# Optimization experiments

Measured on AMD Instinct MI355X. Metric: run time of the kernel, lower is better.

Reference implementation:

```python
import jax, jax.numpy as jnp
import numpy as np
from jax import lax

C = 256          # hidden_channels
K_ITERS = 3      # num_iterations

def _conv(x, w, b, stride=1, pad='SAME'):
    y = lax.conv_general_dilated(x, w, (stride, stride), pad,
                                 dimension_numbers=('NCHW', 'OIHW', 'NCHW'))
    return y + b[None, :, None, None]

def setup_inputs() -> dict:
    key = jax.random.key(0)
    ks = jax.random.split(key, 16)
    B, N, H, W = 1, 3, 384, 384
    def p(k, sh, scale=None):
        if scale is None:
            scale = 1.0 / np.sqrt(np.prod(sh[1:]))
        return jax.random.normal(k, sh, jnp.float32) * scale
    z = lambda: jnp.zeros((C,), jnp.float32)
    return {
        'frames': jax.random.normal(ks[0], (B, N, 3, H, W), jnp.float32),
        'backbone_w': p(ks[1], (C, 3, 8, 8)), 'backbone_b': z(),
        'W_intra': p(ks[2], (C, C), scale=1.0 / C),
        'W_inter': p(ks[3], (C, C), scale=1.0 / C),
        'gate_w': p(ks[4], (C, C, 1, 1)), 'gate_b': z(),
        'Wz': p(ks[5], (C, 2 * C, 3, 3)), 'bz': z(),
        'Wr': p(ks[6], (C, 2 * C, 3, 3)), 'br': z(),
        'Wh': p(ks[7], (C, 2 * C, 3, 3)), 'bh': z(),
        'ro_w1': p(ks[8], (C, 2 * C, 3, 3)), 'ro_b1': z(),
        'ro_w2': p(ks[9], (1, C, 3, 3)), 'ro_b2': jnp.zeros((1,), jnp.float32),
    }

def _forward(frames, backbone_w, backbone_b, W_intra, W_inter, gate_w, gate_b,
             Wz, bz, Wr, br, Wh, bh, ro_w1, ro_b1, ro_w2, ro_b2):
    B, N, _, H, W = frames.shape
    x = frames.reshape(B * N, 3, H, W)
    # backbone: stride-8 conv + ReLU -> node embeddings v (B*N, C, Hf, Wf)
    v = jax.nn.relu(_conv(x, backbone_w, backbone_b, stride=8, pad='VALID'))
    Hf, Wf = v.shape[2], v.shape[3]
    P = Hf * Wf
    v = v.reshape(B, N, C, Hf, Wf)
    h = v
    idx = jnp.arange(N)
    for _ in range(K_ITERS):
        hp = h.reshape(B, N, C, P).transpose(0, 1, 3, 2)      # (B,N,P,C)
        # inter attention e_ij = h_i W h_j^T over all ordered pairs
        t = jnp.einsum('bipc,cd->bipd', hp, W_inter)
        e = jnp.einsum('bipd,bjqd->bijpq', t, hp)              # (B,N,N,P,P)
        # intra (loop-edge) attention on the diagonal, own weight
        ti = jnp.einsum('bipc,cd->bipd', hp, W_intra)
        e_intra = jnp.einsum('bipd,biqd->bipq', ti, hp)        # (B,N,P,P)
        e = e.at[:, idx, idx].set(e_intra)
        attn = jax.nn.softmax(e, axis=-1)
        m = jnp.einsum('bijpq,bjqc->bijpc', attn, hp)          # msg j->i (B,N,N,P,C)
        m = m.transpose(0, 1, 2, 4, 3).reshape(B * N * N, C, Hf, Wf)
        # gated aggregation: sigmoid(1x1 conv) gate, sum over senders j
        g = jax.nn.sigmoid(_conv(m, gate_w, gate_b))
        magg = (g * m).reshape(B, N, N, C, Hf, Wf).sum(axis=2).reshape(B * N, C, Hf, Wf)
        # ConvGRU update
        hflat = h.reshape(B * N, C, Hf, Wf)
        mh = jnp.concatenate([magg, hflat], axis=1)
        zg = jax.nn.sigmoid(_conv(mh, Wz, bz))
        rg = jax.nn.sigmoid(_conv(mh, Wr, br))
        hc = jnp.tanh(_conv(jnp.concatenate([magg, rg * hflat], axis=1), Wh, bh))
        h = ((1.0 - zg) * hflat + zg * hc).reshape(B, N, C, Hf, Wf)
    # read-out on concat(h, v)
    cat = jnp.concatenate([h, v], axis=2).reshape(B * N, 2 * C, Hf, Wf)
    y = jax.nn.relu(_conv(cat, ro_w1, ro_b1))
    masks = _conv(y, ro_w2, ro_b2)
    return masks.reshape(B, N, 1, Hf, Wf)

def reference(frames, backbone_w, backbone_b, W_intra, W_inter, gate_w, gate_b,
              Wz, bz, Wr, br, Wh, bh, ro_w1, ro_b1, ro_w2, ro_b2):
    return _forward(frames, backbone_w, backbone_b, W_intra, W_inter, gate_w, gate_b,
                    Wz, bz, Wr, br, Wh, bh, ro_w1, ro_b1, ro_w2, ro_b2)
```

## Files before the change

kernel.cpp:

```cpp
#include <hip/hip_runtime.h>
#include <hip/hip_bf16.h>
#include <math.h>

#define PIX 2304
#define CCH 256
#define CP  589824
#define NCP 1769472
#define KC  4608
#define PADR 2512

typedef __hip_bfloat16 bf16;
typedef __attribute__((ext_vector_type(8))) short bf16x8;
typedef __attribute__((ext_vector_type(4))) float f32x4;

__device__ __forceinline__ float sigmoidf_(float x){ return 1.f/(1.f+__expf(-x)); }

__device__ __forceinline__ void gl_lds16(const bf16* g, bf16* lds){
    __builtin_amdgcn_global_load_lds(
        (const __attribute__((address_space(1))) void*)g,
        (__attribute__((address_space(3))) void*)lds, 16, 0, 0);
}
#define FENCE() asm volatile("" ::: "memory")

__device__ __forceinline__ float bperm_f(int srcLane, float v){
    return __int_as_float(__builtin_amdgcn_ds_bpermute(srcLane<<2, __float_as_int(v)));
}
__device__ __forceinline__ unsigned packbf(float lo, float hi){
    bf16 a = __float2bfloat16(lo), b = __float2bfloat16(hi);
    return (unsigned)(*(unsigned short*)&a) | ((unsigned)(*(unsigned short*)&b)<<16);
}

__global__ __launch_bounds__(512) void fattn_k(
    const bf16* __restrict__ T, const bf16* __restrict__ Ti,
    const bf16* __restrict__ Khp, const bf16* __restrict__ Vcp,
    bf16* __restrict__ Ob)
{
    __shared__ bf16 Ks[2][64*256];
    __shared__ bf16 Vs[2][256*64];
    __shared__ unsigned Ps[8][512];
    const int z = blockIdx.z, i = z/3, j = z%3;
    const bf16* Q  = ((i==j)? Ti : T) + (long)i*CP;
    const bf16* Kp = Khp + (long)j*CP;
    const bf16* Vp = Vcp + (long)j*CP;
    const int tid = threadIdx.x, l = tid & 63, w = tid >> 6;
    const int g = l>>4, m = l&15;
    const int q0 = blockIdx.x*128;

    bf16x8 qf[8];
    {
        const bf16* qr = Q + (long)(q0 + w*16 + m)*256 + g*8;
        #pragma unroll
        for (int ks=0; ks<8; ++ks) qf[ks] = *(const bf16x8*)(qr + ks*32);
    }
    f32x4 oacc[16];
    #pragma unroll
    for (int nf=0; nf<16; ++nf) oacc[nf] = (f32x4){0.f,0.f,0.f,0.f};
    float mrun = -3e38f;
    float lrun = 0.f;

    auto stage = [&](int buf, int t){
        const int kq = t*64;
        #pragma unroll
        for (int u=0; u<4; ++u){
            int idx = u*512 + tid;
            int rr = idx>>5, cc = idx&31;
            gl_lds16(Kp + (long)(kq+rr)*256 + ((cc ^ (rr&7))<<3),
                     &Ks[buf][(u*512 + (tid & ~63))*8]);
        }
        #pragma unroll
        for (int u=0; u<4; ++u){
            int idx = u*512 + tid;
            int rr = idx>>3, cc = idx&7;
            gl_lds16(Vp + (long)rr*2304 + kq + ((cc ^ (rr&7))<<3),
                     &Vs[buf][(u*512 + (tid & ~63))*8]);
        }
    };

    stage(0, 0);
    int cur = 0;
    char* pw = (char*)&Ps[w][0];
    for (int t=0; t<36; ++t){
        if (t+1 < 36){
            stage(cur^1, t+1);
            asm volatile("s_waitcnt vmcnt(8)" ::: "memory");
        } else {
            asm volatile("s_waitcnt vmcnt(0)" ::: "memory");
        }
        __builtin_amdgcn_s_barrier();
        FENCE();

        f32x4 sacc[4];
        #pragma unroll
        for (int nf=0; nf<4; ++nf) sacc[nf] = (f32x4){0.f,0.f,0.f,0.f};
        __builtin_amdgcn_s_setprio(1);
        #pragma unroll
        for (int ks=0; ks<8; ++ks){
            #pragma unroll
            for (int nf=0; nf<4; ++nf){
                int row = nf*16 + m;
                int phys = (ks*4 + g) ^ (row&7);
                bf16x8 kf = *(const bf16x8*)&Ks[cur][row*256 + phys*8];
                sacc[nf] = __builtin_amdgcn_mfma_f32_16x16x32_bf16(kf, qf[ks], sacc[nf], 0,0,0);
            }
        }
        __builtin_amdgcn_s_setprio(0);

        float pmax = -3e38f;
        #pragma unroll
        for (int nf=0; nf<4; ++nf)
            #pragma unroll
            for (int r=0; r<4; ++r) pmax = fmaxf(pmax, sacc[nf][r]);
        pmax = fmaxf(pmax, __shfl_xor(pmax, 16));
        pmax = fmaxf(pmax, __shfl_xor(pmax, 32));
        if (!__all(pmax - mrun <= 8.f)){
            float mn = fmaxf(mrun, pmax);
            float al = __expf(mrun - mn);
            mrun = mn;
            lrun *= al;
            float ar[4];
            #pragma unroll
            for (int r=0; r<4; ++r) ar[r] = bperm_f((l & 48) | (g*4 + r), al);
            #pragma unroll
            for (int nf=0; nf<16; ++nf)
                #pragma unroll
                for (int r=0; r<4; ++r) oacc[nf][r] *= ar[r];
        }
        float rs = 0.f;
        unsigned pk[4][2];
        #pragma unroll
        for (int nf=0; nf<4; ++nf){
            float p0 = __expf(sacc[nf][0] - mrun);
            float p1 = __expf(sacc[nf][1] - mrun);
            float p2 = __expf(sacc[nf][2] - mrun);
            float p3 = __expf(sacc[nf][3] - mrun);
            rs += (p0+p1) + (p2+p3);
            pk[nf][0] = packbf(p0, p1);
            pk[nf][1] = packbf(p2, p3);
        }
        rs += __shfl_xor(rs, 16);
        rs += __shfl_xor(rs, 32);
        lrun += rs;
        #pragma unroll
        for (int nf=0; nf<4; ++nf)
            #pragma unroll
            for (int s=0; s<2; ++s){
                int ba = m*128 + ((nf*32 + g*8 + s*4) ^ ((m&7)<<4));
                *(unsigned*)(pw + ba) = pk[nf][s];
            }
        asm volatile("s_waitcnt lgkmcnt(0)" ::: "memory");
        __builtin_amdgcn_sched_barrier(0);
        __builtin_amdgcn_s_setprio(1);
        #pragma unroll
        for (int ks2=0; ks2<2; ++ks2){
            bf16x8 pa = *(const bf16x8*)(pw + m*128 + ((ks2*64 + g*16) ^ ((m&7)<<4)));
            #pragma unroll
            for (int nf=0; nf<16; ++nf){
                int row = nf*16 + m;
                int phys = (ks2*4 + g) ^ (row&7);
                bf16x8 bv = *(const bf16x8*)&Vs[cur][row*64 + phys*8];
                oacc[nf] = __builtin_amdgcn_mfma_f32_16x16x32_bf16(pa, bv, oacc[nf], 0,0,0);
            }
        }
        __builtin_amdgcn_s_setprio(0);
        FENCE();
        __builtin_amdgcn_s_barrier();
        FENCE();
        cur ^= 1;
    }

    float linv = 1.f / lrun;
    float li[4];
    #pragma unroll
    for (int r=0; r<4; ++r) li[r] = bperm_f((l & 48) | (g*4 + r), linv);
    bf16* ob = Ob + (long)z*CP;
    const int prow0 = q0 + w*16 + g*4;
    #pragma unroll
    for (int nf=0; nf<16; ++nf){
        int c = nf*16 + m;
        #pragma unroll
        for (int r=0; r<4; ++r)
            ob[(long)(prow0+r)*256 + c] = __float2bfloat16(oacc[nf][r]*li[r]);
    }
}

template<int EPI, int BN>
__global__ __launch_bounds__(256) void mgemm_k(
    const bf16* __restrict__ A0, const bf16* __restrict__ A1, int diagz,
    const bf16* __restrict__ B,
    float* __restrict__ o0, bf16* __restrict__ ob,
    const bf16* __restrict__ aux, const float* __restrict__ bias0,
    int M, int N, int lda, int ldb, int ldc, int auxld,
    long bsA, long bsB, long bsC, long bsAux,
    int nzJ, int Ksub, long bsKc)
{
    __shared__ bf16 As[2][128*64];
    __shared__ bf16 Bs[2][BN*64];
    const int z = blockIdx.z;
    const int jz = z % nzJ, kc = z / nzJ;
    const bf16* Ap = ((jz==diagz)?A1:A0) + jz*bsA + (long)blockIdx.x*128*lda;
    const bf16* Bp = B + jz*bsB + (long)blockIdx.y*BN*ldb;
    const int tid = threadIdx.x, l = tid & 63;
    const int wvu = tid & ~63;
    const int wr = tid>>7, wc = (tid>>6)&1;
    constexpr int NF = BN/32;
    f32x4 acc[4][NF];
    #pragma unroll
    for (int i=0;i<4;++i)
        #pragma unroll
        for (int j=0;j<NF;++j) acc[i][j] = (f32x4){0.f,0.f,0.f,0.f};

    auto stage = [&](int buf, int kb){
        #pragma unroll
        for (int u=0;u<4;++u){
            int idx = u*256 + tid;
            int row = idx>>3, g = (idx&7) ^ (row&7);
            gl_lds16(Ap + (long)row*lda + kb + g*8, &As[buf][(u*256+wvu)*8]);
        }
        #pragma unroll
        for (int u=0;u<BN/32;++u){
            int idx = u*256 + tid;
            int row = idx>>3, g = (idx&7) ^ (row&7);
            gl_lds16(Bp + (long)row*ldb + kb + g*8, &Bs[buf][(u*256+wvu)*8]);
        }
    };

    const int kbeg = kc*Ksub;
    const int nk = Ksub >> 6;
    stage(0, kbeg);
    int cur = 0;
    for (int t=0; t<nk; ++t){
        if (t+1 < nk){
            stage(cur^1, kbeg + (t+1)*64);
            if constexpr (BN==64) asm volatile("s_waitcnt vmcnt(6)" ::: "memory");
            else                  asm volatile("s_waitcnt vmcnt(8)" ::: "memory");
        } else {
            asm volatile("s_waitcnt vmcnt(0)" ::: "memory");
        }
        __builtin_amdgcn_s_barrier();
        FENCE();
        #pragma unroll
        for (int ks=0; ks<64; ks+=32){
            bf16x8 af[4], bfr[NF];
            #pragma unroll
            for (int i=0;i<4;++i){
                int row = wr*64 + i*16 + (l&15);
                af[i] = *(const bf16x8*)&As[cur][row*64 + ((((ks>>3)+(l>>4)) ^ (row&7))<<3)];
            }
            #pragma unroll
            for (int j=0;j<NF;++j){
                int row = wc*(BN/2) + j*16 + (l&15);
                bfr[j] = *(const bf16x8*)&Bs[cur][row*64 + ((((ks>>3)+(l>>4)) ^ (row&7))<<3)];
            }
            #pragma unroll
            for (int i=0;i<4;++i)
                #pragma unroll
                for (int j=0;j<NF;++j)
                    acc[i][j] = __builtin_amdgcn_mfma_f32_16x16x32_bf16(af[i], bfr[j], acc[i][j], 0,0,0);
        }
        FENCE();
        __builtin_amdgcn_s_barrier();
        FENCE();
        cur ^= 1;
    }

    const int mb = blockIdx.x*128 + wr*64, nb = blockIdx.y*BN + wc*(BN/2);
    #pragma unroll
    for (int i=0;i<4;++i)
        #pragma unroll
        for (int j=0;j<NF;++j){
            int gm0 = mb + i*16 + ((l>>4)<<2);
            int gn  = nb + j*16 + (l&15);
            #pragma unroll
            for (int r=0;r<4;++r){
                int gm = gm0 + r;
                float vacc = acc[i][j][r];
                if (EPI==0){
                    ob[jz*bsC + (long)gm*ldc + gn] = __float2bfloat16(vacc);
                } else {
                    float g = sigmoidf_(vacc + bias0[gm]);
                    float mv = __bfloat162float(aux[jz*bsAux + (long)gn*auxld + gm]);
                    o0[jz*bsC + (long)gm*ldc + gn] = g*mv;
                }
            }
        }
}

__global__ __launch_bounds__(256) void cgemm2_k(
    const bf16* __restrict__ inpad, const bf16* __restrict__ W,
    float* __restrict__ part, int N)
{
    __shared__ bf16 As[2][128*64];
    __shared__ bf16 Bs[2][64*64];
    const int tid = threadIdx.x, l = tid & 63, wvu = tid & ~63;
    const int wr = tid>>7, wc = (tid>>6)&1;
    const int bx = blockIdx.x, by = blockIdx.y, kc = blockIdx.z;
    const int img = bx/18, m0 = (bx - img*18)*128;
    const bf16* Ab = inpad + (long)img*PADR*512;
    const bf16* Bb = W + (long)by*64*KC;
    f32x4 acc[4][2];
    #pragma unroll
    for (int i=0;i<4;++i){ acc[i][0]=(f32x4){0,0,0,0}; acc[i][1]=(f32x4){0,0,0,0}; }

    auto stageA = [&](int buf, int k0){
        int tap = k0 >> 9, ci0 = k0 & 511;
        int dy = tap/3, dx = tap - 3*dy;
        int shift = (dy-1)*50 + (dx-1);
        #pragma unroll
        for (int u=0;u<4;++u){
            int idx = u*256 + tid;
            int row = idx>>3;
            int om = m0 + row;
            int prow = om + 2*(om/48) + 51 + shift;
            int g = (idx&7) ^ (row&7);
            gl_lds16(Ab + (long)prow*512 + ci0 + g*8, &As[buf][(u*256+wvu)*8]);
        }
    };
    auto stageB = [&](int buf, int k0){
        #pragma unroll
        for (int u=0;u<2;++u){
            int idx = u*256 + tid;
            int row = idx>>3;
            int g = (idx&7) ^ (row&7);
            gl_lds16(Bb + (long)row*KC + k0 + g*8, &Bs[buf][(u*256+wvu)*8]);
        }
    };

    const int kbeg = kc*2304;
    stageA(0, kbeg); stageB(0, kbeg);
    int cur = 0;
    for (int t=0; t<36; ++t){
        if (t+1 < 36){
            stageA(cur^1, kbeg+(t+1)*64); stageB(cur^1, kbeg+(t+1)*64);
            asm volatile("s_waitcnt vmcnt(6)" ::: "memory");
        } else {
            asm volatile("s_waitcnt vmcnt(0)" ::: "memory");
        }
        __builtin_amdgcn_s_barrier();
        FENCE();
        #pragma unroll
        for (int ks=0; ks<64; ks+=32){
            bf16x8 af[4], bfr[2];
            #pragma unroll
            for (int i=0;i<4;++i){
                int row = wr*64 + i*16 + (l&15);
                af[i] = *(const bf16x8*)&As[cur][row*64 + ((((ks>>3)+(l>>4)) ^ (row&7))<<3)];
            }
            #pragma unroll
            for (int j=0;j<2;++j){
                int row = wc*32 + j*16 + (l&15);
                bfr[j] = *(const bf16x8*)&Bs[cur][row*64 + ((((ks>>3)+(l>>4)) ^ (row&7))<<3)];
            }
            #pragma unroll
            for (int i=0;i<4;++i)
                #pragma unroll
                for (int j=0;j<2;++j)
                    acc[i][j] = __builtin_amdgcn_mfma_f32_16x16x32_bf16(af[i], bfr[j], acc[i][j], 0,0,0);
        }
        FENCE();
        __builtin_amdgcn_s_barrier();
        FENCE();
        cur ^= 1;
    }

    float* pbase = part + (long)kc*N*6912 + (long)img*2304;
    #pragma unroll
    for (int i=0;i<4;++i)
        #pragma unroll
        for (int j=0;j<2;++j){
            int gm0 = m0 + wr*64 + i*16 + ((l>>4)<<2);
            int gn  = by*64 + wc*32 + j*16 + (l&15);
            *(f32x4*)&pbase[(long)gn*6912 + gm0] = acc[i][j];
        }
}

template<int ACT, int DUAL>
__global__ __launch_bounds__(256) void cred_k(const float* __restrict__ part,
        const float* __restrict__ b0, const float* __restrict__ b1,
        float* __restrict__ o0, float* __restrict__ o1,
        const float* __restrict__ hmul, int N)
{
    int id = blockIdx.x*256 + threadIdx.x;
    int c = id / 6912, g = id - c*6912;
    int img = g / 2304, p = g - img*2304;
    float v = part[id] + part[id + (long)N*6912];
    if (DUAL && c >= 256){
        int co = c - 256;
        long oidx = (long)img*CP + (long)co*PIX + p;
        o1[oidx] = sigmoidf_(v + b1[co]) * hmul[oidx];
    } else {
        float r = v + b0[c];
        if (ACT==1) r = sigmoidf_(r);
        else if (ACT==2) r = tanhf(r);
        else r = fmaxf(r, 0.f);
        o0[(long)img*CP + (long)c*PIX + p] = r;
    }
}

__global__ __launch_bounds__(256) void padtr_k(const float* __restrict__ src,
        bf16* __restrict__ dst, int cofs)
{
    __shared__ float tile[64][65];
    const int img = blockIdx.z, p0 = blockIdx.x*64, c0 = blockIdx.y*64;
    const int t = threadIdx.x, tx = t&63, tq = t>>6;
    const float* s = src + (long)img*CP;
    #pragma unroll
    for (int u=0;u<16;++u){
        int r = tq + u*4;
        tile[r][tx] = s[(long)(c0+r)*PIX + p0 + tx];
    }
    __syncthreads();
    bf16* d = dst + (long)img*PADR*512 + cofs + c0;
    #pragma unroll
    for (int u=0;u<16;++u){
        int pl = tq + u*4;
        int p = p0 + pl;
        int prow = p + 2*(p/48) + 51;
        d[(long)prow*512 + tx] = __float2bfloat16(tile[tx][pl]);
    }
}

__global__ __launch_bounds__(256) void convw_k(const float* __restrict__ src,
        bf16* __restrict__ dst, int total)
{
    int idx = blockIdx.x*256 + threadIdx.x;
    if (idx >= total) return;
    int co = idx / KC, r = idx - co*KC;
    int tap = r >> 9, ci = r & 511;
    dst[idx] = __float2bfloat16(src[(long)co*KC + ci*9 + tap]);
}

__global__ __launch_bounds__(256) void prep_h_k(const float* __restrict__ h,
        bf16* __restrict__ hcp, bf16* __restrict__ hp)
{
    __shared__ float tile[64][65];
    const int i = blockIdx.z, p0 = blockIdx.x*64, c0 = blockIdx.y*64;
    const int t = threadIdx.x, tx = t&63, tq = t>>6;
    const float* src = h + (long)i*CP;
    #pragma unroll
    for (int s=0;s<16;++s){
        int r = tq + s*4;
        float v = src[(long)(c0+r)*PIX + p0 + tx];
        tile[r][tx] = v;
        hcp[(long)i*CP + (long)(c0+r)*PIX + p0 + tx] = __float2bfloat16(v);
    }
    __syncthreads();
    #pragma unroll
    for (int s=0;s<16;++s){
        int r = tq + s*4;
        hp[(long)i*CP + (long)(p0+r)*256 + c0 + tx] = __float2bfloat16(tile[tx][r]);
    }
}

__global__ __launch_bounds__(256) void convert_w_k(const float* __restrict__ wint,
    const float* __restrict__ wintra, const float* __restrict__ gw, bf16* __restrict__ o)
{
    int t = blockIdx.x*256 + threadIdx.x;
    int d = t >> 8, c = t & 255;
    o[t]          = __float2bfloat16(wint[c*256 + d]);
    o[65536 + t]  = __float2bfloat16(wintra[c*256 + d]);
    o[131072 + t] = __float2bfloat16(gw[t]);
}

__global__ __launch_bounds__(256) void gatesum_k(const float* __restrict__ g, float* __restrict__ out)
{
    int x = blockIdx.x*256 + threadIdx.x;
    int i = blockIdx.y;
    const float* gi = g + (long)i*3*CP;
    float4 a = ((const float4*)gi)[x];
    float4 b = ((const float4*)gi)[x + CP/4];
    float4 c = ((const float4*)gi)[x + CP/2];
    float4 r; r.x=a.x+b.x+c.x; r.y=a.y+b.y+c.y; r.z=a.z+b.z+c.z; r.w=a.w+b.w+c.w;
    ((float4*)(out + (long)i*CP))[x] = r;
}

__global__ __launch_bounds__(256) void backbone_k(
    const float* __restrict__ frames, const float* __restrict__ W,
    const float* __restrict__ bias, float* __restrict__ v, float* __restrict__ h)
{
    __shared__ float wl[3*64*4];
    const int n = blockIdx.z, o0 = blockIdx.y * 4;
    const int p = blockIdx.x * 256 + threadIdx.x;
    const int y = p / 48, x = p % 48;
    for (int e = threadIdx.x; e < 768; e += 256) {
        int o_sel = e / 192, rem = e % 192, ci = rem / 64, k = rem % 64;
        wl[(ci*64 + k)*4 + o_sel] = W[((long)(o0 + o_sel)*3 + ci)*64 + k];
    }
    __syncthreads();
    float acc[4] = {0.f,0.f,0.f,0.f};
    for (int ci = 0; ci < 3; ++ci) {
        const float* src = frames + (((long)n*3 + ci)*384) * 384;
        #pragma unroll
        for (int k = 0; k < 64; ++k) {
            int ky = k >> 3, kx = k & 7;
            float iv = src[(8*y + ky)*384 + 8*x + kx];
            float4 w = ((const float4*)wl)[ci*64 + k];
            acc[0] += iv*w.x; acc[1] += iv*w.y; acc[2] += iv*w.z; acc[3] += iv*w.w;
        }
    }
    #pragma unroll
    for (int oo = 0; oo < 4; ++oo) {
        float r = fmaxf(acc[oo] + bias[o0 + oo], 0.f);
        long idx = ((long)n*CCH + o0 + oo)*PIX + p;
        v[idx] = r; h[idx] = r;
    }
}

__global__ __launch_bounds__(256) void hupd_k(const float* __restrict__ zg, const float* __restrict__ hc,
                                              float* __restrict__ h)
{
    int idx = blockIdx.x*256 + threadIdx.x;
    float z = zg[idx];
    h[idx] = (1.f - z)*h[idx] + z*hc[idx];
}

__global__ __launch_bounds__(256) void maskpart_k(const float* __restrict__ yin,
        const float* __restrict__ W, float* __restrict__ part)
{
    __shared__ float wl[288];
    const int cb = blockIdx.y * 32;
    for (int e = threadIdx.x; e < 288; e += 256) wl[e] = W[cb*9 + e];
    __syncthreads();
    int id = blockIdx.x*256 + threadIdx.x;
    int n = id / PIX, p = id - n*PIX;
    int y = p / 48, x = p % 48;
    float acc = 0.f;
    for (int ci = 0; ci < 32; ++ci) {
        const float* src = yin + ((long)n*CCH + cb + ci)*PIX;
        #pragma unroll
        for (int dy = 0; dy < 3; ++dy) {
            int yy = y + dy - 1;
            #pragma unroll
            for (int dx = 0; dx < 3; ++dx) {
                int xx = x + dx - 1;
                float iv = (yy >= 0 && yy < 48 && xx >= 0 && xx < 48) ? src[yy*48 + xx] : 0.f;
                acc += iv * wl[ci*9 + dy*3 + dx];
            }
        }
    }
    part[(long)blockIdx.y*(3*PIX) + id] = acc;
}

__global__ __launch_bounds__(256) void maskred_k(const float* __restrict__ part,
        const float* __restrict__ bias, float* __restrict__ out)
{
    int id = blockIdx.x*256 + threadIdx.x;
    float acc = bias[0];
    #pragma unroll
    for (int s = 0; s < 8; ++s) acc += part[(long)s*(3*PIX) + id];
    out[id] = acc;
}

extern "C" void kernel_launch(void* const* d_in, const int* in_sizes, int n_in,
                              void* d_out, int out_size, void* d_ws, size_t ws_size,
                              hipStream_t stream)
{
    const float* frames     = (const float*)d_in[0];
    const float* backbone_w = (const float*)d_in[1];
    const float* backbone_b = (const float*)d_in[2];
    const float* W_intra    = (const float*)d_in[3];
    const float* W_inter    = (const float*)d_in[4];
    const float* gate_w     = (const float*)d_in[5];
    const float* gate_b     = (const float*)d_in[6];
    const float* Wz         = (const float*)d_in[7];
    const float* bz         = (const float*)d_in[8];
    const float* Wr         = (const float*)d_in[9];
    const float* br         = (const float*)d_in[10];
    const float* Wh         = (const float*)d_in[11];
    const float* bh         = (const float*)d_in[12];
    const float* ro_w1      = (const float*)d_in[13];
    const float* ro_b1      = (const float*)d_in[14];
    const float* ro_w2      = (const float*)d_in[15];
    const float* ro_b2      = (const float*)d_in[16];
    float* out = (float*)d_out;
    float* ws  = (float*)d_ws;

    float* h    = ws + 0L*NCP;
    float* v    = ws + 1L*NCP;
    float* magg = ws + 2L*NCP;
    float* zg   = ws + 3L*NCP;
    float* rg   = ws + 4L*NCP;
    float* rhg  = ws + 5L*NCP;
    float* hcmb = ws + 6L*NCP;
    float* S    = ws + 7L*NCP;

    float* Mb9f   = S;
    float* hp16f  = S + 7962624;
    float* hcp16f = hp16f + 884736;
    float* t16f   = hcp16f + 884736;
    float* ti16f  = t16f + 884736;
    float* wbase  = S + 11501568;
    bf16* Wint_t   = (bf16*)wbase;
    bf16* Wintra_t = Wint_t + 65536;
    bf16* gatew16  = Wint_t + 131072;
    bf16* cw16     = (bf16*)(wbase + 98304);
    bf16* inpad    = (bf16*)(wbase + 98304 + 2359296);
    float* maskp   = wbase + 98304 + 2359296 + 1929216;

    bf16* Mb9    = (bf16*)Mb9f;
    bf16* hp16   = (bf16*)hp16f;
    bf16* hcp16  = (bf16*)hcp16f;
    bf16* t16    = (bf16*)t16f;
    bf16* ti16   = (bf16*)ti16f;
    float* hc    = hcmb;
    float* gated = zg;
    float* cpart = Mb9f;

    dim3 b256(256);

    hipMemsetAsync(inpad, 0, 3858432*sizeof(bf16), stream);
    backbone_k<<<dim3(9,64,3), b256, 0, stream>>>(frames, backbone_w, backbone_b, v, h);
    convert_w_k<<<dim3(256), b256, 0, stream>>>(W_inter, W_intra, gate_w, Wint_t);
    convw_k<<<dim3(4608), b256, 0, stream>>>(Wz, cw16, 256*KC);
    convw_k<<<dim3(4608), b256, 0, stream>>>(Wr, cw16 + 256L*KC, 256*KC);
    convw_k<<<dim3(4608), b256, 0, stream>>>(Wh, cw16 + 512L*KC, 256*KC);
    convw_k<<<dim3(4608), b256, 0, stream>>>(ro_w1, cw16 + 768L*KC, 256*KC);

    for (int it = 0; it < 3; ++it) {
        prep_h_k<<<dim3(36,4,3), b256, 0, stream>>>(h, hcp16, hp16);
        mgemm_k<0,64><<<dim3(54,4,2), b256, 0, stream>>>(hp16, hp16, -1, Wint_t,
            nullptr, t16, nullptr, nullptr,
            6912,256, 256,256,256, 0, 0L,65536L,1769472L,0L, 2, 256, 0L);
        fattn_k<<<dim3(18,1,9), dim3(512), 0, stream>>>(t16, ti16, hp16, hcp16, Mb9);
        mgemm_k<2,64><<<dim3(2,36,9), b256, 0, stream>>>(gatew16, gatew16, -1,
            Mb9, gated, nullptr, Mb9, gate_b,
            256,2304, 256,256,PIX, 256, 0L,(long)CP,(long)CP,(long)CP,
            9, 256, 0L);
        gatesum_k<<<dim3(576,3), b256, 0, stream>>>(gated, magg);
        padtr_k<<<dim3(36,4,3), b256, 0, stream>>>(magg, inpad, 0);
        padtr_k<<<dim3(36,4,3), b256, 0, stream>>>(h,    inpad, 256);
        cgemm2_k<<<dim3(54,8,2), b256, 0, stream>>>(inpad, cw16, cpart, 512);
        cred_k<1,1><<<dim3(13824), b256, 0, stream>>>(cpart, bz, br, zg, rhg, h, 512);
        padtr_k<<<dim3(36,4,3), b256, 0, stream>>>(rhg, inpad, 256);
        cgemm2_k<<<dim3(54,4,2), b256, 0, stream>>>(inpad, cw16 + 512L*KC, cpart, 256);
        cred_k<2,0><<<dim3(6912), b256, 0, stream>>>(cpart, bh, nullptr, hc, nullptr, nullptr, 256);
        hupd_k<<<dim3(6912), b256, 0, stream>>>(zg, hc, h);
    }

    padtr_k<<<dim3(36,4,3), b256, 0, stream>>>(h, inpad, 0);
    padtr_k<<<dim3(36,4,3), b256, 0, stream>>>(v, inpad, 256);
    cgemm2_k<<<dim3(54,4,2), b256, 0, stream>>>(inpad, cw16 + 768L*KC, cpart, 256);
    cred_k<3,0><<<dim3(6912), b256, 0, stream>>>(cpart, ro_b1, nullptr, zg, nullptr, nullptr, 256);
    maskpart_k<<<dim3(27,8), b256, 0, stream>>>(zg, ro_w2, maskp);
    maskred_k<<<dim3(27), b256, 0, stream>>>(maskp, ro_b2, out);
}
```

Measured before the change: 949.4 us.

## Split flash attention over keys, widen conv GEMM tiles, fuse GRU update

Flash attention now splits the key range in two across blockIdx.y, writing unnormalized fp32 partial outputs plus running max and sum. A new combine kernel merges the two halves into the bf16 message buffer, which doubles the attention grid from 162 blocks for better CU occupancy, at the cost of extra fp32 traffic and one more launch. The conv GEMM tile grows from 128x64 to 128x128 output to raise reuse and halve the grid. The final cred and hupd kernels are fused into one credh kernel that applies tanh and the GRU blend, removing an intermediate buffer pass.

After: 962.2 us. Within noise of the previous version (+1.4%).

```diff
diff --git a/kernel.cpp b/kernel.cpp
--- a/kernel.cpp
+++ b/kernel.cpp
@@ -8,6 +8,7 @@
 #define NCP 1769472
 #define KC  4608
 #define PADR 2512
+#define ZQ  20736
 
 typedef __hip_bfloat16 bf16;
 typedef __attribute__((ext_vector_type(8))) short bf16x8;
@@ -33,18 +34,19 @@
 __global__ __launch_bounds__(512) void fattn_k(
     const bf16* __restrict__ T, const bf16* __restrict__ Ti,
     const bf16* __restrict__ Khp, const bf16* __restrict__ Vcp,
-    bf16* __restrict__ Ob)
+    float* __restrict__ Op0, float* __restrict__ Op1, float* __restrict__ ml)
 {
     __shared__ bf16 Ks[2][64*256];
     __shared__ bf16 Vs[2][256*64];
     __shared__ unsigned Ps[8][512];
-    const int z = blockIdx.z, i = z/3, j = z%3;
+    const int z = blockIdx.z, i = z/3, j = z%3, kc = blockIdx.y;
     const bf16* Q  = ((i==j)? Ti : T) + (long)i*CP;
     const bf16* Kp = Khp + (long)j*CP;
     const bf16* Vp = Vcp + (long)j*CP;
     const int tid = threadIdx.x, l = tid & 63, w = tid >> 6;
     const int g = l>>4, m = l&15;
     const int q0 = blockIdx.x*128;
+    const int t0 = kc*18;
 
     bf16x8 qf[8];
     {
@@ -76,12 +78,12 @@
         }
     };
 
-    stage(0, 0);
+    stage(0, t0);
     int cur = 0;
     char* pw = (char*)&Ps[w][0];
-    for (int t=0; t<36; ++t){
-        if (t+1 < 36){
-            stage(cur^1, t+1);
+    for (int tt=0; tt<18; ++tt){
+        if (tt+1 < 18){
+            stage(cur^1, t0+tt+1);
             asm volatile("s_waitcnt vmcnt(8)" ::: "memory");
         } else {
             asm volatile("s_waitcnt vmcnt(0)" ::: "memory");
@@ -168,19 +170,40 @@
         cur ^= 1;
     }
 
-    float linv = 1.f / lrun;
-    float li[4];
-    #pragma unroll
-    for (int r=0; r<4; ++r) li[r] = bperm_f((l & 48) | (g*4 + r), linv);
-    bf16* ob = Ob + (long)z*CP;
+    float* Op = (kc ? Op1 : Op0) + (long)z*2304*256;
     const int prow0 = q0 + w*16 + g*4;
     #pragma unroll
     for (int nf=0; nf<16; ++nf){
         int c = nf*16 + m;
         #pragma unroll
         for (int r=0; r<4; ++r)
-            ob[(long)(prow0+r)*256 + c] = __float2bfloat16(oacc[nf][r]*li[r]);
-    }
+            Op[(long)(prow0+r)*256 + c] = oacc[nf][r];
+    }
+    if (g == 0){
+        int q = q0 + w*16 + m;
+        ml[(kc*2+0)*ZQ + z*2304 + q] = mrun;
+        ml[(kc*2+1)*ZQ + z*2304 + q] = lrun;
+    }
+}
+
+__global__ __launch_bounds__(256) void fcomb_k(
+    const float* __restrict__ O0, const float* __restrict__ O1,
+    const float* __restrict__ ml, bf16* __restrict__ Mb9)
+{
+    int id = blockIdx.x*256 + threadIdx.x;
+    int zq = id >> 6;
+    float m0 = ml[zq], l0 = ml[ZQ + zq];
+    float m1 = ml[2*ZQ + zq], l1 = ml[3*ZQ + zq];
+    float M = fmaxf(m0, m1);
+    float a0 = __expf(m0 - M), a1 = __expf(m1 - M);
+    float inv = 1.f / (a0*l0 + a1*l1);
+    a0 *= inv; a1 *= inv;
+    f32x4 o0 = ((const f32x4*)O0)[id];
+    f32x4 o1 = ((const f32x4*)O1)[id];
+    bf16 r[4];
+    #pragma unroll
+    for (int k2=0; k2<4; ++k2) r[k2] = __float2bfloat16(a0*o0[k2] + a1*o1[k2]);
+    *(uint2*)&Mb9[(long)id*4] = *(uint2*)r;
 }
 
 template<int EPI, int BN>
@@ -290,16 +313,18 @@
     float* __restrict__ part, int N)
 {
     __shared__ bf16 As[2][128*64];
-    __shared__ bf16 Bs[2][64*64];
+    __shared__ bf16 Bs[2][128*64];
     const int tid = threadIdx.x, l = tid & 63, wvu = tid & ~63;
     const int wr = tid>>7, wc = (tid>>6)&1;
     const int bx = blockIdx.x, by = blockIdx.y, kc = blockIdx.z;
     const int img = bx/18, m0 = (bx - img*18)*128;
     const bf16* Ab = inpad + (long)img*PADR*512;
-    const bf16* Bb = W + (long)by*64*KC;
-    f32x4 acc[4][2];
-    #pragma unroll
-    for (int i=0;i<4;++i){ acc[i][0]=(f32x4){0,0,0,0}; acc[i][1]=(f32x4){0,0,0,0}; }
+    const bf16* Bb = W + (long)by*128*KC;
+    f32x4 acc[4][4];
+    #pragma unroll
+    for (int i=0;i<4;++i)
+        #pragma unroll
+        for (int j=0;j<4;++j) acc[i][j] = (f32x4){0.f,0.f,0.f,0.f};
 
     auto stageA = [&](int buf, int k0){
         int tap = k0 >> 9, ci0 = k0 & 511;
@@ -317,7 +342,7 @@
     };
     auto stageB = [&](int buf, int k0){
         #pragma unroll
-        for (int u=0;u<2;++u){
+        for (int u=0;u<4;++u){
             int idx = u*256 + tid;
             int row = idx>>3;
             int g = (idx&7) ^ (row&7);
@@ -331,7 +356,7 @@
     for (int t=0; t<36; ++t){
         if (t+1 < 36){
             stageA(cur^1, kbeg+(t+1)*64); stageB(cur^1, kbeg+(t+1)*64);
-            asm volatile("s_waitcnt vmcnt(6)" ::: "memory");
+            asm volatile("s_waitcnt vmcnt(8)" ::: "memory");
         } else {
             asm volatile("s_waitcnt vmcnt(0)" ::: "memory");
         }
@@ -339,21 +364,21 @@
         FENCE();
         #pragma unroll
         for (int ks=0; ks<64; ks+=32){
-            bf16x8 af[4], bfr[2];
+            bf16x8 af[4], bfr[4];
             #pragma unroll
             for (int i=0;i<4;++i){
                 int row = wr*64 + i*16 + (l&15);
                 af[i] = *(const bf16x8*)&As[cur][row*64 + ((((ks>>3)+(l>>4)) ^ (row&7))<<3)];
             }
             #pragma unroll
-            for (int j=0;j<2;++j){
-                int row = wc*32 + j*16 + (l&15);
+            for (int j=0;j<4;++j){
+                int row = wc*64 + j*16 + (l&15);
                 bfr[j] = *(const bf16x8*)&Bs[cur][row*64 + ((((ks>>3)+(l>>4)) ^ (row&7))<<3)];
             }
             #pragma unroll
             for (int i=0;i<4;++i)
                 #pragma unroll
-                for (int j=0;j<2;++j)
+                for (int j=0;j<4;++j)
                     acc[i][j] = __builtin_amdgcn_mfma_f32_16x16x32_bf16(af[i], bfr[j], acc[i][j], 0,0,0);
         }
         FENCE();
@@ -366,9 +391,9 @@
     #pragma unroll
     for (int i=0;i<4;++i)
         #pragma unroll
-        for (int j=0;j<2;++j){
+        for (int j=0;j<4;++j){
             int gm0 = m0 + wr*64 + i*16 + ((l>>4)<<2);
-            int gn  = by*64 + wc*32 + j*16 + (l&15);
+            int gn  = by*128 + wc*64 + j*16 + (l&15);
             *(f32x4*)&pbase[(long)gn*6912 + gm0] = acc[i][j];
         }
 }
@@ -396,6 +421,20 @@
     }
 }
 
+__global__ __launch_bounds__(256) void credh_k(const float* __restrict__ part,
+        const float* __restrict__ bh, const float* __restrict__ zg,
+        float* __restrict__ h)
+{
+    int id = blockIdx.x*256 + threadIdx.x;
+    int c = id / 6912, g = id - c*6912;
+    int img = g / 2304, p = g - img*2304;
+    float v = part[id] + part[id + 256L*6912];
+    float hcv = tanhf(v + bh[c]);
+    long oidx = (long)img*CP + (long)c*PIX + p;
+    float z = zg[oidx];
+    h[oidx] = (1.f - z)*h[oidx] + z*hcv;
+}
+
 __global__ __launch_bounds__(256) void padtr_k(const float* __restrict__ src,
         bf16* __restrict__ dst, int cofs)
 {
@@ -503,14 +542,6 @@
         long idx = ((long)n*CCH + o0 + oo)*PIX + p;
         v[idx] = r; h[idx] = r;
     }
-}
-
-__global__ __launch_bounds__(256) void hupd_k(const float* __restrict__ zg, const float* __restrict__ hc,
-                                              float* __restrict__ h)
-{
-    int idx = blockIdx.x*256 + threadIdx.x;
-    float z = zg[idx];
-    h[idx] = (1.f - z)*h[idx] + z*hc[idx];
 }
 
 __global__ __launch_bounds__(256) void maskpart_k(const float* __restrict__ yin,
@@ -601,9 +632,11 @@
     bf16* hcp16  = (bf16*)hcp16f;
     bf16* t16    = (bf16*)t16f;
     bf16* ti16   = (bf16*)ti16f;
-    float* hc    = hcmb;
-    float* gated = zg;
-    float* cpart = Mb9f;
+    float* Opart0 = zg;
+    float* Opart1 = Mb9f + 2654208;
+    float* mlbuf  = hcmb;
+    float* gated  = zg;
+    float* cpart  = Mb9f;
 
     dim3 b256(256);
 
@@ -620,7 +653,9 @@
         mgemm_k<0,64><<<dim3(54,4,2), b256, 0, stream>>>(hp16, hp16, -1, Wint_t,
             nullptr, t16, nullptr, nullptr,
             6912,256, 256,256,256, 0, 0L,65536L,1769472L,0L, 2, 256, 0L);
-        fattn_k<<<dim3(18,1,9), dim3(512), 0, stream>>>(t16, ti16, hp16, hcp16, Mb9);
+        fattn_k<<<dim3(18,2,9), dim3(512), 0, stream>>>(t16, ti16, hp16, hcp16,
+            Opart0, Opart1, mlbuf);
+        fcomb_k<<<dim3(5184), b256, 0, stream>>>(Opart0, Opart1, mlbuf, Mb9);
         mgemm_k<2,64><<<dim3(2,36,9), b256, 0, stream>>>(gatew16, gatew16, -1,
             Mb9, gated, nullptr, Mb9, gate_b,
             256,2304, 256,256,PIX, 256, 0L,(long)CP,(long)CP,(long)CP,
@@ -628,17 +663,16 @@
         gatesum_k<<<dim3(576,3), b256, 0, stream>>>(gated, magg);
         padtr_k<<<dim3(36,4,3), b256, 0, stream>>>(magg, inpad, 0);
         padtr_k<<<dim3(36,4,3), b256, 0, stream>>>(h,    inpad, 256);
-        cgemm2_k<<<dim3(54,8,2), b256, 0, stream>>>(inpad, cw16, cpart, 512);
+        cgemm2_k<<<dim3(54,4,2), b256, 0, stream>>>(inpad, cw16, cpart, 512);
         cred_k<1,1><<<dim3(13824), b256, 0, stream>>>(cpart, bz, br, zg, rhg, h, 512);
         padtr_k<<<dim3(36,4,3), b256, 0, stream>>>(rhg, inpad, 256);
-        cgemm2_k<<<dim3(54,4,2), b256, 0, stream>>>(inpad, cw16 + 512L*KC, cpart, 256);
-        cred_k<2,0><<<dim3(6912), b256, 0, stream>>>(cpart, bh, nullptr, hc, nullptr, nullptr, 256);
-        hupd_k<<<dim3(6912), b256, 0, stream>>>(zg, hc, h);
+        cgemm2_k<<<dim3(54,2,2), b256, 0, stream>>>(inpad, cw16 + 512L*KC, cpart, 256);
+        credh_k<<<dim3(6912), b256, 0, stream>>>(cpart, bh, zg, h);
     }
 
     padtr_k<<<dim3(36,4,3), b256, 0, stream>>>(h, inpad, 0);
     padtr_k<<<dim3(36,4,3), b256, 0, stream>>>(v, inpad, 256);
-    cgemm2_k<<<dim3(54,4,2), b256, 0, stream>>>(inpad, cw16 + 768L*KC, cpart, 256);
+    cgemm2_k<<<dim3(54,2,2), b256, 0, stream>>>(inpad, cw16 + 768L*KC, cpart, 256);
     cred_k<3,0><<<dim3(6912), b256, 0, stream>>>(cpart, ro_b1, nullptr, zg, nullptr, nullptr, 256);
     maskpart_k<<<dim3(27,8), b256, 0, stream>>>(zg, ro_w2, maskp);
     maskred_k<<<dim3(27), b256, 0, stream>>>(maskp, ro_b2, out);
```
